# Kernel optimization log

Measured on AMD Instinct MI355X. Metric: run time of the kernel, lower is better.

The kernel has to match this reference:

```python
import jax, jax.numpy as jnp
import numpy as np

N, B, DIM, H, K = 4096, 4, 1024, 16, 64
DH = DIM // H

def setup_inputs() -> dict:
    key = jax.random.key(0)
    ks = jax.random.split(key, 7)
    s = 1.0 / np.sqrt(DIM)
    return {
        "x": jax.random.normal(ks[0], (N, B, DIM), dtype=jnp.float32),
        "E": jax.random.normal(ks[1], (N, K), dtype=jnp.float32),
        "F": jax.random.normal(ks[2], (N, K), dtype=jnp.float32),
        "W_qkv": jax.random.uniform(ks[3], (DIM, 3 * DIM), dtype=jnp.float32, minval=-s, maxval=s),
        "b_qkv": jax.random.uniform(ks[4], (3 * DIM,), dtype=jnp.float32, minval=-s, maxval=s),
        "W_out": jax.random.uniform(ks[5], (DIM, DIM), dtype=jnp.float32, minval=-s, maxval=s),
        "b_out": jax.random.uniform(ks[6], (DIM,), dtype=jnp.float32, minval=-s, maxval=s),
    }

def reference(x, E, F, W_qkv, b_qkv, W_out, b_out):
    n, b, _ = x.shape
    qkv = x @ W_qkv + b_qkv                      # (n, b, 3*dim)
    q, k, v = jnp.split(qkv, 3, axis=-1)
    # (n, b, dim) -> (b, h, n, dh)
    to_bhnd = lambda t: t.reshape(n, b, H, DH).transpose(1, 2, 0, 3)
    q, k, v = to_bhnd(q), to_bhnd(k), to_bhnd(v)
    k = jnp.einsum('bhnd,nk->bhkd', k, E)        # low-rank K: (b, h, K, dh)
    v = jnp.einsum('bhnd,nk->bhkd', v, F)
    scale = DH ** -0.5
    dots = jnp.einsum('bhnd,bhkd->bhnk', q, k) * scale
    attn = jax.nn.softmax(dots, axis=-1)
    out = jnp.einsum('bhnk,bhkd->bhnd', attn, v)
    out = out.transpose(2, 0, 1, 3).reshape(n, b, DIM)
    return out @ W_out + b_out
```

## Files before the change

kernel.cpp:

```cpp
#include <hip/hip_runtime.h>

#define DIMN 4096
#define DIMB 4
#define DIMH 16
#define DIMK 64
#define DH   64

typedef __attribute__((ext_vector_type(8))) __bf16 bf16x8;
typedef __attribute__((ext_vector_type(8))) _Float16 f16x8;
typedef __attribute__((ext_vector_type(8))) unsigned short u16x8;
typedef __attribute__((ext_vector_type(4))) float f32x4;
typedef __attribute__((ext_vector_type(4))) int i32x4;

__device__ __forceinline__ unsigned short f2bf(float f) {
  union { float f; unsigned u; } v; v.f = f;
  unsigned r = v.u + 0x7FFFu + ((v.u >> 16) & 1u);
  return (unsigned short)(r >> 16);
}
__device__ __forceinline__ float bf2f(unsigned short u) {
  union { unsigned u; float f; } v; v.u = ((unsigned)u) << 16; return v.f;
}
__device__ __forceinline__ void split2(float f, unsigned short& h, unsigned short& l) {
  h = f2bf(f);
  l = f2bf(f - bf2f(h));
}
__device__ __forceinline__ unsigned short f2h(float f) {
  _Float16 h = (_Float16)f;
  return __builtin_bit_cast(unsigned short, h);
}
__device__ __forceinline__ bf16x8 ldbf8(const unsigned short* p) {
  return __builtin_bit_cast(bf16x8, *(const u16x8*)p);
}
__device__ __forceinline__ f16x8 ldh8(const unsigned short* p) {
  return __builtin_bit_cast(f16x8, *(const u16x8*)p);
}
__device__ __forceinline__ f32x4 mfma16(bf16x8 a, bf16x8 b, f32x4 c) {
  return __builtin_amdgcn_mfma_f32_16x16x32_bf16(a, b, c, 0, 0, 0);
}
__device__ __forceinline__ f32x4 mfma16h(f16x8 a, f16x8 b, f32x4 c) {
  return __builtin_amdgcn_mfma_f32_16x16x32_f16(a, b, c, 0, 0, 0);
}

__device__ __forceinline__ void gl_lds16(const unsigned short* g, unsigned short* l) {
  __builtin_amdgcn_global_load_lds(
      (const __attribute__((address_space(1))) unsigned int*)g,
      (__attribute__((address_space(3))) unsigned int*)l, 16, 0, 0);
}

__device__ __forceinline__ void stage_tile(const unsigned short* src, int stride,
                                           unsigned short* lds, int tid, int k0) {
  const int wave = tid >> 6;
  #pragma unroll
  for (int s = 0; s < 2; ++s) {
    int idx = tid + s * 256;
    int row = idx >> 2;
    int slot = idx & 3;
    gl_lds16(&src[(size_t)row * stride + k0 + ((slot ^ (row & 3)) * 8)],
             &lds[(size_t)(s * 256 + wave * 64) * 8]);
  }
}
__device__ __forceinline__ const unsigned short* frag_ptr(const unsigned short* lds,
                                                          int row, int quad) {
  return &lds[row * 32 + ((quad ^ (row & 3)) * 8)];
}

__global__ void transpose_cast(const float* __restrict__ src, unsigned short* __restrict__ dst,
                               int R, int C) {
  __shared__ float tile[32][33];
  int c0 = blockIdx.x * 32, r0 = blockIdx.y * 32;
  for (int i = threadIdx.y; i < 32; i += 8)
    tile[i][threadIdx.x] = src[(size_t)(r0 + i) * C + c0 + threadIdx.x];
  __syncthreads();
  for (int i = threadIdx.y; i < 32; i += 8)
    dst[(size_t)(c0 + i) * R + r0 + threadIdx.x] = f2bf(tile[threadIdx.x][i]);
}

__global__ void transpose_wq_f16(const float* __restrict__ W, unsigned short* __restrict__ t) {
  __shared__ float tile[32][33];
  int c0 = blockIdx.x * 32, r0 = blockIdx.y * 32;
  for (int i = threadIdx.y; i < 32; i += 8)
    tile[i][threadIdx.x] = W[(size_t)(r0 + i) * 3072 + c0 + threadIdx.x];
  __syncthreads();
  for (int i = threadIdx.y; i < 32; i += 8)
    t[(size_t)(c0 + i) * 1024 + r0 + threadIdx.x] = f2h(tile[threadIdx.x][i]);
}

__global__ void transpose_split_wkv(const float* __restrict__ W,
                                    unsigned short* __restrict__ th,
                                    unsigned short* __restrict__ tl) {
  __shared__ float tile[32][33];
  int c0 = blockIdx.x * 32, r0 = blockIdx.y * 32;
  for (int i = threadIdx.y; i < 32; i += 8)
    tile[i][threadIdx.x] = W[(size_t)(r0 + i) * 3072 + 1024 + c0 + threadIdx.x];
  __syncthreads();
  for (int i = threadIdx.y; i < 32; i += 8) {
    float v = tile[threadIdx.x][i];
    unsigned short h, l; split2(v, h, l);
    size_t o = (size_t)(c0 + i) * 1024 + r0 + threadIdx.x;
    th[o] = h;
    tl[o] = l;
  }
}

__global__ void transpose_EF_f16(const float* __restrict__ E, const float* __restrict__ F,
                                 unsigned short* __restrict__ t) {
  __shared__ float tile[32][33];
  const float* src = blockIdx.z ? F : E;
  const int kkbase = blockIdx.z * 64;
  int c0 = blockIdx.x * 32, r0 = blockIdx.y * 32;
  for (int i = threadIdx.y; i < 32; i += 8)
    tile[i][threadIdx.x] = src[(size_t)(r0 + i) * 64 + c0 + threadIdx.x];
  __syncthreads();
  for (int i = threadIdx.y; i < 32; i += 8)
    t[(size_t)(kkbase + c0 + i) * 4096 + r0 + threadIdx.x] = f2h(tile[threadIdx.x][i]);
}

__global__ __launch_bounds__(256) void cast_x_f16(
    const float* __restrict__ src, unsigned short* __restrict__ d) {
  const int total4 = DIMN * DIMB * 1024 / 4;
  int i = blockIdx.x * 256 + threadIdx.x;
  const int stride = gridDim.x * 256;
  for (; i < total4; i += stride) {
    float4 v = ((const float4*)src)[i];
    ushort4 h;
    h.x = f2h(v.x); h.y = f2h(v.y); h.z = f2h(v.z); h.w = f2h(v.w);
    ((ushort4*)d)[i] = h;
  }
}

__global__ __launch_bounds__(256) void gemm_q_f16(
    const unsigned short* __restrict__ A, const unsigned short* __restrict__ Bt,
    const float* __restrict__ bias, unsigned short* __restrict__ q)
{
  __shared__ unsigned short As[128 * 32];
  __shared__ unsigned short Bs[128 * 32];
  const int tid  = threadIdx.x;
  const int wave = tid >> 6, lane = tid & 63;
  const int quad = lane >> 4, l16 = lane & 15;
  const int wm = (wave >> 1) * 64, wn = (wave & 1) * 64;
  const int m0 = blockIdx.x * 128, n0 = blockIdx.y * 128;
  const unsigned short* Ab = A  + (size_t)m0 * 1024;
  const unsigned short* Bb = Bt + (size_t)n0 * 1024;

  f32x4 acc[4][4] = {};

  for (int k0 = 0; k0 < 1024; k0 += 32) {
    stage_tile(Ab, 1024, As, tid, k0);
    stage_tile(Bb, 1024, Bs, tid, k0);
    __syncthreads();
    f16x8 af[4], bfr[4];
    #pragma unroll
    for (int i = 0; i < 4; ++i) af[i]  = ldh8(frag_ptr(As, wm + 16 * i + l16, quad));
    #pragma unroll
    for (int j = 0; j < 4; ++j) bfr[j] = ldh8(frag_ptr(Bs, wn + 16 * j + l16, quad));
    #pragma unroll
    for (int i = 0; i < 4; ++i)
      #pragma unroll
      for (int j = 0; j < 4; ++j)
        acc[i][j] = mfma16h(af[i], bfr[j], acc[i][j]);
    __syncthreads();
  }

  #pragma unroll
  for (int i = 0; i < 4; ++i)
    #pragma unroll
    for (int j = 0; j < 4; ++j) {
      int col = n0 + wn + 16 * j + l16;
      float bs = bias[col];
      int h = col >> 6, d = col & 63;
      #pragma unroll
      for (int r = 0; r < 4; ++r) {
        int row = m0 + wm + 16 * i + quad * 4 + r;
        int n = row >> 2, b = row & 3;
        q[(((size_t)(b * DIMH + h) * DIMN + n) << 6) + d] = f2bf(acc[i][j][r] + bs);
      }
    }
}

__global__ __launch_bounds__(256) void gemm_xEF(
    const unsigned short* __restrict__ xf, const unsigned short* __restrict__ ef,
    float* __restrict__ partial)
{
  __shared__ unsigned short Ash[128 * 40];
  __shared__ unsigned short Bsh[128 * 40];
  const int tid  = threadIdx.x;
  const int wave = tid >> 6, lane = tid & 63;
  const int quad = lane >> 4, l16 = lane & 15;
  const int wm = (wave >> 1) * 64, wn = (wave & 1) * 64;
  const int c0 = blockIdx.x * 128;
  const int ks = blockIdx.y;

  f32x4 acc[4][4] = {};

  const int kend = ks * 512 + 512;
  for (int k0 = ks * 512; k0 < kend; k0 += 32) {
    #pragma unroll
    for (int s = 0; s < 2; ++s) {
      int idx = tid + s * 256;
      int row = idx >> 2;
      int kc  = (idx & 3) * 8;
      *(i32x4*)&Ash[row * 40 + kc] = *(const i32x4*)&ef[(size_t)row * 4096 + k0 + kc];
    }
    #pragma unroll
    for (int s = 0; s < 2; ++s) {
      int n_l = tid & 31;
      int c8  = (tid >> 5) + s * 8;
      u16x8 vh = *(const u16x8*)&xf[(size_t)(k0 + n_l) * 4096 + c0 + c8 * 8];
      #pragma unroll
      for (int e = 0; e < 8; ++e)
        Bsh[(c8 * 8 + e) * 40 + n_l] = vh[e];
    }
    __syncthreads();
    f16x8 afh[4], bfh[4];
    #pragma unroll
    for (int i = 0; i < 4; ++i) afh[i] = ldh8(&Ash[(wm + 16 * i + l16) * 40 + quad * 8]);
    #pragma unroll
    for (int j = 0; j < 4; ++j) bfh[j] = ldh8(&Bsh[(wn + 16 * j + l16) * 40 + quad * 8]);
    #pragma unroll
    for (int i = 0; i < 4; ++i)
      #pragma unroll
      for (int j = 0; j < 4; ++j)
        acc[i][j] = mfma16h(afh[i], bfh[j], acc[i][j]);
    __syncthreads();
  }

  #pragma unroll
  for (int i = 0; i < 4; ++i)
    #pragma unroll
    for (int j = 0; j < 4; ++j) {
      int col = c0 + wn + 16 * j + l16;
      #pragma unroll
      for (int r = 0; r < 4; ++r) {
        int m = wm + 16 * i + quad * 4 + r;
        partial[((size_t)ks * 128 + m) * 4096 + col] = acc[i][j][r];
      }
    }
}

__global__ __launch_bounds__(256) void reduce_xEF2(
    const float* __restrict__ partial, unsigned short* __restrict__ xh,
    unsigned short* __restrict__ xl)
{
  int t_lin = blockIdx.x * 256 + threadIdx.x;
  float s = 0.f;
  #pragma unroll
  for (int ks = 0; ks < 8; ++ks)
    s += partial[(size_t)ks * 524288 + t_lin];
  int kk = t_lin >> 12, c = t_lin & 4095;
  int t = kk >> 6, kkl = kk & 63, b = c >> 10, k = c & 1023;
  int m = t * 256 + b * 64 + kkl;
  unsigned short h, l; split2(s, h, l);
  xh[m * 1024 + k] = h;
  xl[m * 1024 + k] = l;
}

__global__ __launch_bounds__(256) void colsum_EF1(
    const float* __restrict__ E, const float* __restrict__ F,
    float* __restrict__ partS)
{
  const int src = blockIdx.x;
  const int ch  = blockIdx.y;
  const float* S = src ? F : E;
  const int r  = threadIdx.x >> 6;
  const int kk = threadIdx.x & 63;
  const int n0 = ch * 256;
  float s = 0.f;
  #pragma unroll 8
  for (int i = 0; i < 64; ++i)
    s += S[(size_t)(n0 + r + 4 * i) * 64 + kk];
  __shared__ float red[4][64];
  red[r][kk] = s;
  __syncthreads();
  if (r == 0)
    partS[((size_t)src * 16 + ch) * 64 + kk] = red[0][kk] + red[1][kk] + red[2][kk] + red[3][kk];
}

__global__ void colsum_EF2(const float* __restrict__ partS, float* __restrict__ sEF) {
  int t = threadIdx.x;
  int src = t >> 6, kk = t & 63;
  float s = 0.f;
  #pragma unroll
  for (int ch = 0; ch < 16; ++ch)
    s += partS[((size_t)src * 16 + ch) * 64 + kk];
  sEF[t] = s;
}

__global__ __launch_bounds__(256) void gemm_klv(
    const unsigned short* __restrict__ Ah, const unsigned short* __restrict__ Al,
    const unsigned short* __restrict__ Bh, const unsigned short* __restrict__ Bl,
    const float* __restrict__ bias, const float* __restrict__ sEF,
    float* __restrict__ klow, float* __restrict__ vlow)
{
  __shared__ unsigned short Ash[128 * 32], Asl[128 * 32];
  __shared__ unsigned short Bsh[128 * 32], Bsl[128 * 32];
  const int tid  = threadIdx.x;
  const int wave = tid >> 6, lane = tid & 63;
  const int quad = lane >> 4, l16 = lane & 15;
  const int wm = (wave >> 1) * 64, wn = (wave & 1) * 64;
  const int mt = blockIdx.y;
  const int t  = mt >> 1;
  const int m0 = mt * 128;
  const int n0 = blockIdx.x * 128;
  const int brow = t * 1024 + n0;
  const unsigned short* Ahb = Ah + (size_t)m0 * 1024;
  const unsigned short* Alb = Al + (size_t)m0 * 1024;
  const unsigned short* Bhb = Bh + (size_t)brow * 1024;
  const unsigned short* Blb = Bl + (size_t)brow * 1024;

  f32x4 acc[4][4] = {};

  for (int k0 = 0; k0 < 1024; k0 += 32) {
    stage_tile(Ahb, 1024, Ash, tid, k0);
    stage_tile(Alb, 1024, Asl, tid, k0);
    stage_tile(Bhb, 1024, Bsh, tid, k0);
    stage_tile(Blb, 1024, Bsl, tid, k0);
    __syncthreads();
    bf16x8 afh[4], afl[4], bfh[4], bfl[4];
    #pragma unroll
    for (int i = 0; i < 4; ++i) {
      afh[i] = ldbf8(frag_ptr(Ash, wm + 16 * i + l16, quad));
      afl[i] = ldbf8(frag_ptr(Asl, wm + 16 * i + l16, quad));
    }
    #pragma unroll
    for (int j = 0; j < 4; ++j) {
      bfh[j] = ldbf8(frag_ptr(Bsh, wn + 16 * j + l16, quad));
      bfl[j] = ldbf8(frag_ptr(Bsl, wn + 16 * j + l16, quad));
    }
    #pragma unroll
    for (int i = 0; i < 4; ++i)
      #pragma unroll
      for (int j = 0; j < 4; ++j) {
        acc[i][j] = mfma16(afh[i], bfh[j], acc[i][j]);
        acc[i][j] = mfma16(afh[i], bfl[j], acc[i][j]);
        acc[i][j] = mfma16(afl[i], bfh[j], acc[i][j]);
      }
    __syncthreads();
  }

  float* dstb = (t ? vlow : klow);
  #pragma unroll
  for (int i = 0; i < 4; ++i)
    #pragma unroll
    for (int j = 0; j < 4; ++j) {
      int c = n0 + wn + 16 * j + l16;
      int h = c >> 6, d = c & 63;
      float bs = bias[1024 * (1 + t) + c];
      #pragma unroll
      for (int r = 0; r < 4; ++r) {
        int m = m0 + wm + 16 * i + quad * 4 + r;
        int b = (m >> 6) & 3, kk = m & 63;
        float val = acc[i][j][r] + sEF[t * 64 + kk] * bs;
        dstb[(((size_t)b * DIMH + h) * DIMK + kk) * DH + d] = val;
      }
    }
}

__global__ __launch_bounds__(256) void attn_fused(
    const unsigned short* __restrict__ qb, const float* __restrict__ klow,
    const float* __restrict__ vlow, unsigned short* __restrict__ ctx)
{
  __shared__ unsigned short VTh[64][72], VTl[64][72];
  __shared__ unsigned short Plds[4][32][72];
  const int bh = blockIdx.x, b = bh >> 4, h = bh & 15;
  const unsigned short* Q  = qb   + (size_t)bh * DIMN * DH;
  const float* KL = klow + (size_t)bh * DIMK * DH;
  const float* VL = vlow + (size_t)bh * DIMK * DH;
  const int tid = threadIdx.x, wave = tid >> 6, lane = tid & 63;
  const int quad = lane >> 4, l16 = lane & 15;

  #pragma unroll
  for (int it = 0; it < 2; ++it) {
    int idx = tid + it * 256;
    int kk = idx >> 3, d0 = (idx & 7) * 8;
    float4 f0 = *(const float4*)&VL[kk * DH + d0];
    float4 f1 = *(const float4*)&VL[kk * DH + d0 + 4];
    float vv[8] = {f0.x, f0.y, f0.z, f0.w, f1.x, f1.y, f1.z, f1.w};
    #pragma unroll
    for (int e = 0; e < 8; ++e) {
      unsigned short hh, ll;
      split2(vv[e], hh, ll);
      VTh[d0 + e][kk] = hh;
      VTl[d0 + e][kk] = ll;
    }
  }
  bf16x8 kfh[2][4], kfl[2][4];
  #pragma unroll
  for (int dc = 0; dc < 2; ++dc)
    #pragma unroll
    for (int j = 0; j < 4; ++j) {
      const float* p = &KL[(j * 16 + l16) * DH + dc * 32 + quad * 8];
      float4 f0 = *(const float4*)p;
      float4 f1 = *(const float4*)(p + 4);
      float vv[8] = {f0.x, f0.y, f0.z, f0.w, f1.x, f1.y, f1.z, f1.w};
      alignas(16) unsigned short th[8], tl[8];
      #pragma unroll
      for (int e = 0; e < 8; ++e) split2(vv[e], th[e], tl[e]);
      kfh[dc][j] = ldbf8(th);
      kfl[dc][j] = ldbf8(tl);
    }
  __syncthreads();

  const int n_base = blockIdx.y * 128 + wave * 32;

  f32x4 sacc[2][4] = {};
  #pragma unroll
  for (int rt = 0; rt < 2; ++rt)
    #pragma unroll
    for (int dc = 0; dc < 2; ++dc) {
      bf16x8 a = ldbf8(&Q[(size_t)(n_base + rt * 16 + l16) * DH + dc * 32 + quad * 8]);
      #pragma unroll
      for (int j = 0; j < 4; ++j) {
        sacc[rt][j] = mfma16(a, kfh[dc][j], sacc[rt][j]);
        sacc[rt][j] = mfma16(a, kfl[dc][j], sacc[rt][j]);
      }
    }

  const float scale = 0.125f;
  #pragma unroll
  for (int rt = 0; rt < 2; ++rt)
    #pragma unroll
    for (int r = 0; r < 4; ++r) {
      float v0 = sacc[rt][0][r] * scale, v1 = sacc[rt][1][r] * scale;
      float v2 = sacc[rt][2][r] * scale, v3 = sacc[rt][3][r] * scale;
      float mx = fmaxf(fmaxf(v0, v1), fmaxf(v2, v3));
      #pragma unroll
      for (int off = 1; off < 16; off <<= 1)
        mx = fmaxf(mx, __shfl_xor(mx, off, 64));
      float e0 = __expf(v0 - mx), e1 = __expf(v1 - mx);
      float e2 = __expf(v2 - mx), e3 = __expf(v3 - mx);
      float sm = e0 + e1 + e2 + e3;
      #pragma unroll
      for (int off = 1; off < 16; off <<= 1)
        sm += __shfl_xor(sm, off, 64);
      float inv = 1.0f / sm;
      int prow = rt * 16 + quad * 4 + r;
      Plds[wave][prow][ 0 + l16] = f2bf(e0 * inv);
      Plds[wave][prow][16 + l16] = f2bf(e1 * inv);
      Plds[wave][prow][32 + l16] = f2bf(e2 * inv);
      Plds[wave][prow][48 + l16] = f2bf(e3 * inv);
    }
  __syncthreads();

  f32x4 oacc[2][4] = {};
  #pragma unroll
  for (int rt = 0; rt < 2; ++rt)
    #pragma unroll
    for (int kc = 0; kc < 2; ++kc) {
      bf16x8 a = ldbf8(&Plds[wave][rt * 16 + l16][kc * 32 + quad * 8]);
      #pragma unroll
      for (int j = 0; j < 4; ++j) {
        bf16x8 bh_ = ldbf8(&VTh[j * 16 + l16][kc * 32 + quad * 8]);
        bf16x8 bl_ = ldbf8(&VTl[j * 16 + l16][kc * 32 + quad * 8]);
        oacc[rt][j] = mfma16(a, bh_, oacc[rt][j]);
        oacc[rt][j] = mfma16(a, bl_, oacc[rt][j]);
      }
    }

  #pragma unroll
  for (int rt = 0; rt < 2; ++rt)
    #pragma unroll
    for (int j = 0; j < 4; ++j)
      #pragma unroll
      for (int r = 0; r < 4; ++r) {
        int n = n_base + rt * 16 + quad * 4 + r;
        ctx[((size_t)(n * DIMB + b) << 10) + h * DH + j * 16 + l16] = f2bf(oacc[rt][j][r]);
      }
}

__global__ __launch_bounds__(256) void gemm128_out(
    const unsigned short* __restrict__ A, const unsigned short* __restrict__ Bt,
    const float* __restrict__ bias, float* __restrict__ outF)
{
  __shared__ unsigned short As[128 * 32];
  __shared__ unsigned short Bs[128 * 32];
  const int tid  = threadIdx.x;
  const int wave = tid >> 6, lane = tid & 63;
  const int quad = lane >> 4, l16 = lane & 15;
  const int wm = (wave >> 1) * 64, wn = (wave & 1) * 64;
  const int m0 = blockIdx.x * 128, n0 = blockIdx.y * 128;
  const unsigned short* Ab = A  + (size_t)m0 * 1024;
  const unsigned short* Bb = Bt + (size_t)n0 * 1024;

  f32x4 acc[4][4] = {};

  for (int k0 = 0; k0 < 1024; k0 += 32) {
    stage_tile(Ab, 1024, As, tid, k0);
    stage_tile(Bb, 1024, Bs, tid, k0);
    __syncthreads();
    bf16x8 af[4], bfr[4];
    #pragma unroll
    for (int i = 0; i < 4; ++i) af[i]  = ldbf8(frag_ptr(As, wm + 16 * i + l16, quad));
    #pragma unroll
    for (int j = 0; j < 4; ++j) bfr[j] = ldbf8(frag_ptr(Bs, wn + 16 * j + l16, quad));
    #pragma unroll
    for (int i = 0; i < 4; ++i)
      #pragma unroll
      for (int j = 0; j < 4; ++j)
        acc[i][j] = mfma16(af[i], bfr[j], acc[i][j]);
    __syncthreads();
  }

  #pragma unroll
  for (int i = 0; i < 4; ++i)
    #pragma unroll
    for (int j = 0; j < 4; ++j) {
      int col = n0 + wn + 16 * j + l16;
      float bs = bias[col];
      #pragma unroll
      for (int r = 0; r < 4; ++r) {
        int row = m0 + wm + 16 * i + quad * 4 + r;
        outF[(size_t)row * 1024 + col] = acc[i][j][r] + bs;
      }
    }
}

extern "C" void kernel_launch(void* const* d_in, const int* in_sizes, int n_in,
                              void* d_out, int out_size, void* d_ws, size_t ws_size,
                              hipStream_t stream) {
  const float* x    = (const float*)d_in[0];
  const float* E    = (const float*)d_in[1];
  const float* F    = (const float*)d_in[2];
  const float* Wqkv = (const float*)d_in[3];
  const float* bqkv = (const float*)d_in[4];
  const float* Wout = (const float*)d_in[5];
  const float* bout = (const float*)d_in[6];
  float* out = (float*)d_out;

  const size_t MB = 1024 * 1024;
  char* ws = (char*)d_ws;
  unsigned short* qb    = (unsigned short*)ws;
  float*          partQ = (float*)ws;
  unsigned short* xf16  = (unsigned short*)(ws + 32 * MB);
  unsigned short* ctx   = (unsigned short*)(ws + 32 * MB);
  unsigned short* wqT   = (unsigned short*)(ws + 64 * MB);
  unsigned short* WoutT = (unsigned short*)(ws + 66 * MB);
  unsigned short* eft   = (unsigned short*)(ws + 68 * MB);
  unsigned short* xEFh  = (unsigned short*)(ws + 69 * MB);
  unsigned short* xEFl  = (unsigned short*)(ws + 70 * MB);
  unsigned short* wkvh  = (unsigned short*)(ws + 71 * MB);
  unsigned short* wkvl  = (unsigned short*)(ws + 75 * MB);
  float*          sEF   = (float*)(ws + 79 * MB);
  float*          klow  = (float*)(ws + 79 * MB + 65536);
  float*          vlow  = (float*)(ws + 80 * MB + 65536);
  float*          partS = (float*)(ws + 81 * MB + 65536);

  transpose_wq_f16<<<dim3(32, 32), dim3(32, 8), 0, stream>>>(Wqkv, wqT);
  cast_x_f16<<<dim3(2048), dim3(256), 0, stream>>>(x, xf16);
  transpose_EF_f16<<<dim3(2, 128, 2), dim3(32, 8), 0, stream>>>(E, F, eft);
  transpose_split_wkv<<<dim3(64, 32), dim3(32, 8), 0, stream>>>(Wqkv, wkvh, wkvl);
  gemm_xEF<<<dim3(32, 8), dim3(256), 0, stream>>>(xf16, eft, partQ);
  reduce_xEF2<<<dim3(2048), dim3(256), 0, stream>>>(partQ, xEFh, xEFl);
  colsum_EF1<<<dim3(2, 16), dim3(256), 0, stream>>>(E, F, partS);
  colsum_EF2<<<dim3(1), dim3(128), 0, stream>>>(partS, sEF);
  gemm_klv<<<dim3(8, 4), dim3(256), 0, stream>>>(xEFh, xEFl, wkvh, wkvl, bqkv, sEF, klow, vlow);

  gemm_q_f16<<<dim3(128, 8), dim3(256), 0, stream>>>(xf16, wqT, bqkv, qb);

  transpose_cast<<<dim3(32, 32), dim3(32, 8), 0, stream>>>(Wout, WoutT, 1024, 1024);
  attn_fused<<<dim3(64, 32), dim3(256), 0, stream>>>(qb, klow, vlow, ctx);
  gemm128_out<<<dim3(128, 8), dim3(256), 0, stream>>>(ctx, WoutT, bout, out);
}
```

Baseline: 361.4 us.

## Double-buffer LDS tiles in Q and output GEMMs and change the swizzle

The Q-projection and output-projection GEMMs now use two LDS buffers per operand. The next K-slice is issued with global_load_lds right after the current fragments are read, so the global load overlaps the MFMA work and one barrier per iteration is removed. The LDS swizzle XOR key also changes from row&3 to (row>>1)&3, which is meant to reduce bank conflicts on the 16-byte fragment reads. LDS use doubles, which may lower occupancy. Correctness also depends on the async loads completing before the single barrier.

```diff
diff --git a/kernel.cpp b/kernel.cpp
--- a/kernel.cpp
+++ b/kernel.cpp
@@ -55,13 +55,13 @@
     int idx = tid + s * 256;
     int row = idx >> 2;
     int slot = idx & 3;
-    gl_lds16(&src[(size_t)row * stride + k0 + ((slot ^ (row & 3)) * 8)],
+    gl_lds16(&src[(size_t)row * stride + k0 + ((slot ^ ((row >> 1) & 3)) * 8)],
              &lds[(size_t)(s * 256 + wave * 64) * 8]);
   }
 }
 __device__ __forceinline__ const unsigned short* frag_ptr(const unsigned short* lds,
                                                           int row, int quad) {
-  return &lds[row * 32 + ((quad ^ (row & 3)) * 8)];
+  return &lds[row * 32 + ((quad ^ ((row >> 1) & 3)) * 8)];
 }
 
 __global__ void transpose_cast(const float* __restrict__ src, unsigned short* __restrict__ dst,
@@ -132,8 +132,8 @@
     const unsigned short* __restrict__ A, const unsigned short* __restrict__ Bt,
     const float* __restrict__ bias, unsigned short* __restrict__ q)
 {
-  __shared__ unsigned short As[128 * 32];
-  __shared__ unsigned short Bs[128 * 32];
+  __shared__ unsigned short As0[128 * 32], As1[128 * 32];
+  __shared__ unsigned short Bs0[128 * 32], Bs1[128 * 32];
   const int tid  = threadIdx.x;
   const int wave = tid >> 6, lane = tid & 63;
   const int quad = lane >> 4, l16 = lane & 15;
@@ -144,21 +144,31 @@
 
   f32x4 acc[4][4] = {};
 
-  for (int k0 = 0; k0 < 1024; k0 += 32) {
-    stage_tile(Ab, 1024, As, tid, k0);
-    stage_tile(Bb, 1024, Bs, tid, k0);
-    __syncthreads();
+  stage_tile(Ab, 1024, As0, tid, 0);
+  stage_tile(Bb, 1024, Bs0, tid, 0);
+  __syncthreads();
+  int cur = 0;
+  for (int t = 0; t < 32; ++t) {
+    const unsigned short* Ac = cur ? As1 : As0;
+    const unsigned short* Bc = cur ? Bs1 : Bs0;
+    unsigned short* An = cur ? As0 : As1;
+    unsigned short* Bn = cur ? Bs0 : Bs1;
     f16x8 af[4], bfr[4];
     #pragma unroll
-    for (int i = 0; i < 4; ++i) af[i]  = ldh8(frag_ptr(As, wm + 16 * i + l16, quad));
-    #pragma unroll
-    for (int j = 0; j < 4; ++j) bfr[j] = ldh8(frag_ptr(Bs, wn + 16 * j + l16, quad));
+    for (int i = 0; i < 4; ++i) af[i]  = ldh8(frag_ptr(Ac, wm + 16 * i + l16, quad));
+    #pragma unroll
+    for (int j = 0; j < 4; ++j) bfr[j] = ldh8(frag_ptr(Bc, wn + 16 * j + l16, quad));
+    if (t < 31) {
+      stage_tile(Ab, 1024, An, tid, (t + 1) * 32);
+      stage_tile(Bb, 1024, Bn, tid, (t + 1) * 32);
+    }
     #pragma unroll
     for (int i = 0; i < 4; ++i)
       #pragma unroll
       for (int j = 0; j < 4; ++j)
         acc[i][j] = mfma16h(af[i], bfr[j], acc[i][j]);
-    __syncthreads();
+    if (t < 31) __syncthreads();
+    cur ^= 1;
   }
 
   #pragma unroll
@@ -471,8 +481,8 @@
     const unsigned short* __restrict__ A, const unsigned short* __restrict__ Bt,
     const float* __restrict__ bias, float* __restrict__ outF)
 {
-  __shared__ unsigned short As[128 * 32];
-  __shared__ unsigned short Bs[128 * 32];
+  __shared__ unsigned short As0[128 * 32], As1[128 * 32];
+  __shared__ unsigned short Bs0[128 * 32], Bs1[128 * 32];
   const int tid  = threadIdx.x;
   const int wave = tid >> 6, lane = tid & 63;
   const int quad = lane >> 4, l16 = lane & 15;
@@ -483,21 +493,31 @@
 
   f32x4 acc[4][4] = {};
 
-  for (int k0 = 0; k0 < 1024; k0 += 32) {
-    stage_tile(Ab, 1024, As, tid, k0);
-    stage_tile(Bb, 1024, Bs, tid, k0);
-    __syncthreads();
+  stage_tile(Ab, 1024, As0, tid, 0);
+  stage_tile(Bb, 1024, Bs0, tid, 0);
+  __syncthreads();
+  int cur = 0;
+  for (int t = 0; t < 32; ++t) {
+    const unsigned short* Ac = cur ? As1 : As0;
+    const unsigned short* Bc = cur ? Bs1 : Bs0;
+    unsigned short* An = cur ? As0 : As1;
+    unsigned short* Bn = cur ? Bs0 : Bs1;
     bf16x8 af[4], bfr[4];
     #pragma unroll
-    for (int i = 0; i < 4; ++i) af[i]  = ldbf8(frag_ptr(As, wm + 16 * i + l16, quad));
-    #pragma unroll
-    for (int j = 0; j < 4; ++j) bfr[j] = ldbf8(frag_ptr(Bs, wn + 16 * j + l16, quad));
+    for (int i = 0; i < 4; ++i) af[i]  = ldbf8(frag_ptr(Ac, wm + 16 * i + l16, quad));
+    #pragma unroll
+    for (int j = 0; j < 4; ++j) bfr[j] = ldbf8(frag_ptr(Bc, wn + 16 * j + l16, quad));
+    if (t < 31) {
+      stage_tile(Ab, 1024, An, tid, (t + 1) * 32);
+      stage_tile(Bb, 1024, Bn, tid, (t + 1) * 32);
+    }
     #pragma unroll
     for (int i = 0; i < 4; ++i)
       #pragma unroll
       for (int j = 0; j < 4; ++j)
         acc[i][j] = mfma16(af[i], bfr[j], acc[i][j]);
-    __syncthreads();
+    if (t < 31) __syncthreads();
+    cur ^= 1;
   }
 
   #pragma unroll
```

Result: no change. 368.2 us (+1.9%).
